# Kernel optimization log

Hardware: AMD Instinct MI355X
Metric: run time of the kernel (lower is better)

Reference implementation:

```python
import jax, jax.numpy as jnp
import numpy as np

REACH = 2
BS = 32  # blocksize
NHID = 15  # nlayers - 1
CI = 12    # 2*(reach+1)*reach


def _offsets():
    # matches get_nb ordering: rows above (dy=-2,-1; dx=-2..2), then left (dy=0; dx=-2,-1)
    offs = [(dy, dx) for dy in range(-REACH, 0) for dx in range(-REACH, REACH + 1)]
    offs += [(0, dx) for dx in range(-REACH, 0)]
    return offs


def setup_inputs() -> dict:
    key = jax.random.key(0)
    k0, k1, k2, k3, k4 = jax.random.split(key, 5)
    x = jax.random.uniform(k0, (8, 3, 512, 512), jnp.float32, -1.0, 1.0)
    s = 1.0 / np.sqrt(CI).astype(np.float32)
    Wh = jax.random.uniform(k1, (NHID, CI, CI), jnp.float32, -s, s)
    bh = jax.random.uniform(k2, (NHID, CI), jnp.float32, -s, s)
    Wo = jax.random.uniform(k3, (1, CI), jnp.float32, -s, s)
    bo = jax.random.uniform(k4, (1,), jnp.float32, -s, s)
    return {"x": x, "Wh": Wh, "bh": bh, "Wo": Wo, "bo": bo}


def reference(x, Wh, bh, Wo, bo):
    b, c, h, w = x.shape
    h = h // BS * BS
    w = w // BS * BS
    x = x[:, :, :h, :w]
    nbh, nbw = h // BS, w // BS
    # unfold into (nbc, BS, BS) blocks, matching torch unfold/unfold/reshape
    blocks = x.reshape(b, c, nbh, BS, nbw, BS).transpose(0, 1, 2, 4, 3, 5).reshape(-1, BS, BS)
    xp = jnp.pad(blocks, ((0, 0), (REACH, REACH), (REACH, REACH)))
    # batched causal-neighbor gather: (nbc, BS, BS, 12)
    feats = jnp.stack(
        [xp[:, REACH + dy:REACH + dy + BS, REACH + dx:REACH + dx + BS] for dy, dx in _offsets()],
        axis=-1,
    )
    hdn = feats
    for l in range(NHID):
        hdn = jax.nn.leaky_relu(jnp.einsum('nhwi,oi->nhwo', hdn, Wh[l]) + bh[l])
    pred = jnp.clip(jnp.einsum('nhwi,oi->nhwo', hdn, Wo)[..., 0] + bo[0], -1.0, 1.0)
    deltas = jnp.fmod(blocks - pred + 1.0, 2.0) - 1.0
    deltas = deltas.reshape(b * c, h * w)
    loss1 = 255.0 * jnp.sqrt(jnp.mean(jnp.square(deltas)))
    return (loss1, deltas)
```

## Files before the change

### kernel.cpp

```cpp
#include <hip/hip_runtime.h>
#include <math.h>

#define CI 12
#define NHID 15
#define NBLK 6144
#define GRID 1024
#define ITERS 6
#define NPIX (NBLK * 1024)
#define TSZ (36 * 37)

typedef int i32x2 __attribute__((ext_vector_type(2)));

static __device__ __forceinline__ int h2pack(float lo, float hi) {
    auto h = __builtin_amdgcn_cvt_pkrtz(lo, hi);
    int r;
    __builtin_memcpy(&r, &h, 4);
    return r;
}

#define LKA \
  "v_cvt_pkrtz_f16_f32 v36, v44, v45\n" \
  "v_cvt_pkrtz_f16_f32 v37, v46, v47\n" \
  "v_pk_mul_f16 v60, s21, v36\n" \
  "v_pk_mul_f16 v61, s21, v37\n" \
  "v_pk_max_f16 v36, v36, v60\n" \
  "v_pk_max_f16 v37, v37, v61\n"
#define LKB \
  "v_cvt_pkrtz_f16_f32 v38, v48, v49\n" \
  "v_cvt_pkrtz_f16_f32 v39, v50, v51\n" \
  "v_pk_mul_f16 v60, s21, v38\n" \
  "v_pk_mul_f16 v61, s21, v39\n" \
  "v_pk_max_f16 v38, v38, v60\n" \
  "v_pk_max_f16 v39, v39, v61\n"
#define LKC \
  "v_cvt_pkrtz_f16_f32 v40, v52, v53\n" \
  "v_cvt_pkrtz_f16_f32 v41, v54, v55\n" \
  "v_pk_mul_f16 v60, s21, v40\n" \
  "v_pk_mul_f16 v61, s21, v41\n" \
  "v_pk_max_f16 v40, v40, v60\n" \
  "v_pk_max_f16 v41, v41, v61\n"
#define LKD \
  "v_cvt_pkrtz_f16_f32 v42, v56, v57\n" \
  "v_cvt_pkrtz_f16_f32 v43, v58, v59\n" \
  "v_pk_mul_f16 v60, s21, v42\n" \
  "v_pk_mul_f16 v61, s21, v43\n" \
  "v_pk_max_f16 v42, v42, v60\n" \
  "v_pk_max_f16 v43, v43, v61\n"

#define MFA(w) "v_mfma_f32_16x16x16_f16 v[44:47], %[" w "], v[36:37], v[32:35]\n"
#define MFB(w) "v_mfma_f32_16x16x16_f16 v[48:51], %[" w "], v[38:39], v[32:35]\n"
#define MFC(w) "v_mfma_f32_16x16x16_f16 v[52:55], %[" w "], v[40:41], v[32:35]\n"
#define MFD(w) "v_mfma_f32_16x16x16_f16 v[56:59], %[" w "], v[42:43], v[32:35]\n"

#define LAYER(w) LKA LKB MFA(w) LKC MFB(w) LKD MFC(w) "s_nop 1\n" MFD(w)

__global__ __launch_bounds__(256, 4) void codec_main(
    const float* __restrict__ x,
    const float* __restrict__ Wh,
    const float* __restrict__ bh,
    const float* __restrict__ Wo,
    const float* __restrict__ bo,
    float* __restrict__ out,
    float* __restrict__ loss_acc)
{
    __shared__ float tile[2][TSZ];
    __shared__ float stage[4][256];
    __shared__ float wsum[4];

    const int bid  = blockIdx.x;
    const int tid  = threadIdx.x;
    const int lane = tid & 63;
    const int wv   = tid >> 6;
    const int t    = lane & 15;
    const int q    = lane >> 4;
    const int col  = tid & 31;
    const int r0   = tid >> 5;

    #pragma unroll
    for (int i = 0; i < 11; ++i) {
        int idx = tid + i * 256;
        if (idx < 2 * TSZ) ((float*)tile)[idx] = 0.0f;
    }

    i32x2 wq[16];
    #pragma unroll
    for (int l = 0; l < NHID; ++l) {
        int w0 = 0, w1 = 0;
        if (q < 3 && t < CI) {
            float4 w = *(const float4*)(Wh + l * (CI * CI) + t * CI + 4 * q);
            w0 = h2pack(w.x, w.y);
            w1 = h2pack(w.z, w.w);
        }
        if (q == 3 && t < CI)  w0 = h2pack(bh[l * CI + t], 0.f);
        if (q == 3 && t == CI) w0 = 0x3C00;
        wq[l] = (i32x2){ w0, w1 };
    }
    {
        int w0 = 0, w1 = 0;
        if (t == 0 && q < 3) {
            float4 w = *(const float4*)(Wo + 4 * q);
            w0 = h2pack(w.x, w.y);
            w1 = h2pack(w.z, w.w);
        }
        if (t == 0 && q == 3) w0 = h2pack(bo[0], 0.f);
        wq[15] = (i32x2){ w0, w1 };
    }

    const int sh8  = q * 8;
    const int off0 = (int)(signed char)((0x00DCB8B4u >> sh8) & 0xFFu);
    const int off1 = (int)(signed char)((0x00DDD9B5u >> sh8) & 0xFFu);
    const int off2 = (int)(signed char)((0x00FEDAB6u >> sh8) & 0xFFu);
    const int off3 = (int)(signed char)((0x00FFDBB7u >> sh8) & 0xFFu);
    const bool q3  = (q == 3);

    __syncthreads();

    {
        const int bc = bid >> 8, blk = bid & 255, by = blk >> 4, bx = blk & 15;
        #pragma unroll
        for (int p = 0; p < 4; ++p) {
            const int row = r0 + 8 * p;
            tile[0][(row + 2) * 37 + col + 2] =
                x[((size_t)bc * 512 + (size_t)(by * 32 + row)) * 512
                  + (size_t)(bx * 32 + col)];
        }
    }
    __syncthreads();

    const int ebase = (wv * 8 + 2) * 37 + (t + 2);
    float d2 = 0.0f;

    #pragma unroll 1
    for (int it = 0; it < ITERS; ++it) {
        const int cur = it & 1;
        const float* tl = &tile[cur][0];
        const int n = bid + it * GRID;

        int e = ebase;
        #pragma unroll 1
        for (int yi = 0; yi < 4; ++yi) {
            const int faA0 = q3 ? 0x3C00 : h2pack(tl[e + off0],      tl[e + off1]);
            const int faA1 = q3 ? 0      : h2pack(tl[e + off2],      tl[e + off3]);
            const int fbA0 = q3 ? 0x3C00 : h2pack(tl[e + off0 + 16], tl[e + off1 + 16]);
            const int fbA1 = q3 ? 0      : h2pack(tl[e + off2 + 16], tl[e + off3 + 16]);
            const int fcA0 = q3 ? 0x3C00 : h2pack(tl[e + off0 + 37], tl[e + off1 + 37]);
            const int fcA1 = q3 ? 0      : h2pack(tl[e + off2 + 37], tl[e + off3 + 37]);
            const int fdA0 = q3 ? 0x3C00 : h2pack(tl[e + off0 + 53], tl[e + off1 + 53]);
            const int fdA1 = q3 ? 0      : h2pack(tl[e + off2 + 53], tl[e + off3 + 53]);
            const float vA = tl[e], vB = tl[e + 16];
            const float vC = tl[e + 37], vD = tl[e + 53];

            float pA, pB, pC, pD;
            asm volatile(
                "s_mov_b32 s21, 0x211f211f\n"
                "v_mov_b32 v32, 0\n" "v_mov_b32 v33, 0\n"
                "v_mov_b32 v34, 0\n" "v_mov_b32 v35, 0\n"
                "v_mov_b32 v36, %[fa0]\n" "v_mov_b32 v37, %[fa1]\n"
                "v_mov_b32 v38, %[fb0]\n" "v_mov_b32 v39, %[fb1]\n"
                "v_mov_b32 v40, %[fc0]\n" "v_mov_b32 v41, %[fc1]\n"
                "v_mov_b32 v42, %[fd0]\n" "v_mov_b32 v43, %[fd1]\n"
                MFA("w0") MFB("w0") MFC("w0") MFD("w0")
                "s_nop 7\n" "s_nop 7\n" "s_nop 7\n" "s_nop 4\n"
                LAYER("w1")  LAYER("w2")  LAYER("w3")  LAYER("w4")
                LAYER("w5")  LAYER("w6")  LAYER("w7")  LAYER("w8")
                LAYER("w9")  LAYER("w10") LAYER("w11") LAYER("w12")
                LAYER("w13") LAYER("w14") LAYER("w15")
                "v_mov_b32 %[pA], v44\n"
                "s_nop 1\n"
                "v_mov_b32 %[pB], v48\n"
                "s_nop 7\n" "s_nop 7\n"
                "v_mov_b32 %[pC], v52\n"
                "s_nop 3\n"
                "v_mov_b32 %[pD], v56\n"
                : [pA] "=v"(pA), [pB] "=v"(pB), [pC] "=v"(pC), [pD] "=v"(pD)
                : [w0] "a"(wq[0]),  [w1] "a"(wq[1]),  [w2] "a"(wq[2]),
                  [w3] "a"(wq[3]),  [w4] "a"(wq[4]),  [w5] "a"(wq[5]),
                  [w6] "a"(wq[6]),  [w7] "a"(wq[7]),  [w8] "a"(wq[8]),
                  [w9] "a"(wq[9]),  [w10] "a"(wq[10]), [w11] "a"(wq[11]),
                  [w12] "a"(wq[12]), [w13] "a"(wq[13]), [w14] "a"(wq[14]),
                  [w15] "a"(wq[15]),
                  [fa0] "v"(faA0), [fa1] "v"(faA1), [fb0] "v"(fbA0), [fb1] "v"(fbA1),
                  [fc0] "v"(fcA0), [fc1] "v"(fcA1), [fd0] "v"(fdA0), [fd1] "v"(fdA1)
                : "s21",
                  "v32","v33","v34","v35","v36","v37","v38","v39",
                  "v40","v41","v42","v43","v44","v45","v46","v47",
                  "v48","v49","v50","v51","v52","v53","v54","v55",
                  "v56","v57","v58","v59","v60","v61");

            if (lane < 16) {
                const float qA = fminf(fmaxf(pA, -1.0f), 1.0f);
                const float uA = vA - qA + 1.0f;
                const float dA = uA - ((uA < 2.0f) ? 1.0f : 3.0f);
                const float qB = fminf(fmaxf(pB, -1.0f), 1.0f);
                const float uB = vB - qB + 1.0f;
                const float dB = uB - ((uB < 2.0f) ? 1.0f : 3.0f);
                const float qC = fminf(fmaxf(pC, -1.0f), 1.0f);
                const float uC = vC - qC + 1.0f;
                const float dC = uC - ((uC < 2.0f) ? 1.0f : 3.0f);
                const float qD = fminf(fmaxf(pD, -1.0f), 1.0f);
                const float uD = vD - qD + 1.0f;
                const float dD = uD - ((uD < 2.0f) ? 1.0f : 3.0f);
                const int r = 2 * yi;
                stage[wv][r * 32 + t]            = dA;
                stage[wv][r * 32 + 16 + t]       = dB;
                stage[wv][(r + 1) * 32 + t]      = dC;
                stage[wv][(r + 1) * 32 + 16 + t] = dD;
                d2 = fmaf(dA, dA, fmaf(dB, dB, fmaf(dC, dC, fmaf(dD, dD, d2))));
            }
            e += 74;
        }

        float* outp = out + 1 + (size_t)n * 1024 + wv * 256;
        #pragma unroll
        for (int j = 0; j < 4; ++j)
            outp[j * 64 + lane] = stage[wv][j * 64 + lane];

        if (it + 1 < ITERS) {
            const int nn = n + GRID;
            const int bc = nn >> 8, blk = nn & 255, by = blk >> 4, bx = blk & 15;
            const float* xp = x + ((size_t)bc * 512 + (size_t)(by * 32 + r0)) * 512
                                + (size_t)(bx * 32 + col);
            float* nt = &tile[cur ^ 1][0];
            nt[(r0 + 2)  * 37 + col + 2] = xp[0];
            nt[(r0 + 10) * 37 + col + 2] = xp[8 * 512];
            nt[(r0 + 18) * 37 + col + 2] = xp[16 * 512];
            nt[(r0 + 26) * 37 + col + 2] = xp[24 * 512];
            __syncthreads();
        }
    }

    #pragma unroll
    for (int off = 8; off > 0; off >>= 1) d2 += __shfl_down(d2, off, 64);
    if (lane == 0) wsum[wv] = d2;
    __syncthreads();
    if (tid == 0) atomicAdd(loss_acc, wsum[0] + wsum[1] + wsum[2] + wsum[3]);
}

__global__ void codec_loss(const float* __restrict__ acc, float* __restrict__ out)
{
    out[0] = 255.0f * sqrtf(acc[0] / (float)NPIX);
}

extern "C" void kernel_launch(void* const* d_in, const int* in_sizes, int n_in,
                              void* d_out, int out_size, void* d_ws, size_t ws_size,
                              hipStream_t stream)
{
    const float* x  = (const float*)d_in[0];
    const float* Wh = (const float*)d_in[1];
    const float* bh = (const float*)d_in[2];
    const float* Wo = (const float*)d_in[3];
    const float* bo = (const float*)d_in[4];
    float* out = (float*)d_out;
    float* acc = (float*)d_ws;

    hipMemsetAsync(acc, 0, sizeof(float), stream);
    codec_main<<<GRID, 256, 0, stream>>>(x, Wh, bh, Wo, bo, out, acc);
    codec_loss<<<1, 1, 0, stream>>>(acc, out);
}
```

Measured before the change: 184.8 us.

## Give each wave a private halo strip to remove block-wide barriers

Each wave now stages its own 12-row strip (its 8 output rows plus a 2-row causal halo) of the input block into a per-wave LDS double buffer, instead of the whole block cooperatively filling one shared 36x37 tile. This removes the __syncthreads after every block load, so waves can run their MFMA layer chains independently without waiting on each other. In exchange it adds redundant global loads for halo rows (12 rows per wave instead of 8), slightly more LDS, and relies on wave-level execution to order each wave's LDS writes before its own reads.

```diff
diff --git a/kernel.cpp b/kernel.cpp
--- a/kernel.cpp
+++ b/kernel.cpp
@@ -7,7 +7,8 @@
 #define GRID 1024
 #define ITERS 6
 #define NPIX (NBLK * 1024)
-#define TSZ (36 * 37)
+#define SROW 12
+#define SSZ (SROW * 37)
 
 typedef int i32x2 __attribute__((ext_vector_type(2)));
 
@@ -63,7 +64,7 @@
     float* __restrict__ out,
     float* __restrict__ loss_acc)
 {
-    __shared__ float tile[2][TSZ];
+    __shared__ float strip[4][2][SSZ];
     __shared__ float stage[4][256];
     __shared__ float wsum[4];
 
@@ -73,13 +74,13 @@
     const int wv   = tid >> 6;
     const int t    = lane & 15;
     const int q    = lane >> 4;
-    const int col  = tid & 31;
-    const int r0   = tid >> 5;
+    const int col  = lane & 31;
+    const int kh   = lane >> 5;
 
     #pragma unroll
-    for (int i = 0; i < 11; ++i) {
-        int idx = tid + i * 256;
-        if (idx < 2 * TSZ) ((float*)tile)[idx] = 0.0f;
+    for (int i = 0; i < 14; ++i) {
+        int idx = lane + i * 64;
+        if (idx < 2 * SSZ) (&strip[wv][0][0])[idx] = 0.0f;
     }
 
     i32x2 wq[16];
@@ -113,27 +114,29 @@
     const int off3 = (int)(signed char)((0x00FFDBB7u >> sh8) & 0xFFu);
     const bool q3  = (q == 3);
 
-    __syncthreads();
-
-    {
-        const int bc = bid >> 8, blk = bid & 255, by = blk >> 4, bx = blk & 15;
+    auto stage_strip = [&](int buf, int n) {
+        const int bc = n >> 8, blk = n & 255, by = blk >> 4, bx = blk & 15;
+        const float* xp = x + ((size_t)bc * 512 + (size_t)(by * 32)) * 512
+                            + (size_t)(bx * 32 + col);
+        float* sp = &strip[wv][buf][0];
         #pragma unroll
-        for (int p = 0; p < 4; ++p) {
-            const int row = r0 + 8 * p;
-            tile[0][(row + 2) * 37 + col + 2] =
-                x[((size_t)bc * 512 + (size_t)(by * 32 + row)) * 512
-                  + (size_t)(bx * 32 + col)];
-        }
-    }
-    __syncthreads();
-
-    const int ebase = (wv * 8 + 2) * 37 + (t + 2);
+        for (int s = 0; s < 6; ++s) {
+            const int k  = 2 * s + kh;
+            const int gr = 8 * wv - 2 + k;
+            if ((unsigned)gr < 32u)
+                sp[k * 37 + col + 2] = xp[(size_t)gr * 512];
+        }
+    };
+
+    stage_strip(0, bid);
+
+    const int ebase = 2 * 37 + (t + 2);
     float d2 = 0.0f;
 
     #pragma unroll 1
     for (int it = 0; it < ITERS; ++it) {
         const int cur = it & 1;
-        const float* tl = &tile[cur][0];
+        const float* tl = &strip[wv][cur][0];
         const int n = bid + it * GRID;
 
         int e = ebase;
@@ -215,18 +218,8 @@
         for (int j = 0; j < 4; ++j)
             outp[j * 64 + lane] = stage[wv][j * 64 + lane];
 
-        if (it + 1 < ITERS) {
-            const int nn = n + GRID;
-            const int bc = nn >> 8, blk = nn & 255, by = blk >> 4, bx = blk & 15;
-            const float* xp = x + ((size_t)bc * 512 + (size_t)(by * 32 + r0)) * 512
-                                + (size_t)(bx * 32 + col);
-            float* nt = &tile[cur ^ 1][0];
-            nt[(r0 + 2)  * 37 + col + 2] = xp[0];
-            nt[(r0 + 10) * 37 + col + 2] = xp[8 * 512];
-            nt[(r0 + 18) * 37 + col + 2] = xp[16 * 512];
-            nt[(r0 + 26) * 37 + col + 2] = xp[24 * 512];
-            __syncthreads();
-        }
+        if (it + 1 < ITERS)
+            stage_strip(cur ^ 1, n + GRID);
     }
 
     #pragma unroll
```

Measured after the change: 190.3 us. 1.03x slower.
